# Performance work log

Hardware: AMD Instinct MI355X
Metric: run time of the kernel (lower is better)

## Reference

```python
import jax, jax.numpy as jnp
import numpy as np


def _proj(x, w, b):
    # 1x1 conv as channel matmul: x (n,c,h,w), w (k,c), b (k,) -> (n,k,h,w)
    return jnp.einsum('nchw,kc->nkhw', x, w) + b[None, :, None, None]


def setup_inputs() -> dict:
    key = jax.random.key(0)
    ks = jax.random.split(key, 9)
    cin, cinter = 256, 128
    n, h, w = 4, 64, 64
    s = lambda fan_in: 1.0 / np.sqrt(fan_in)
    return {
        'x': jax.random.normal(ks[0], (n, cin, h, w), jnp.float32),
        'theta_w': jax.random.normal(ks[1], (cinter, cin), jnp.float32) * s(cin),
        'theta_b': jax.random.normal(ks[2], (cinter,), jnp.float32) * 0.01,
        'phi_w': jax.random.normal(ks[3], (cinter, cin), jnp.float32) * s(cin),
        'phi_b': jax.random.normal(ks[4], (cinter,), jnp.float32) * 0.01,
        'g_w': jax.random.normal(ks[5], (cinter, cin), jnp.float32) * s(cin),
        'g_b': jax.random.normal(ks[6], (cinter,), jnp.float32) * 0.01,
        'w_w': jax.random.normal(ks[7], (cin, cinter), jnp.float32) * s(cinter),
        'w_b': jax.random.normal(ks[8], (cin,), jnp.float32) * 0.01,
    }


def reference(x, theta_w, theta_b, phi_w, phi_b, g_w, g_b, w_w, w_b):
    n, c, h, w = x.shape
    cinter = theta_w.shape[0]
    hw = h * w
    theta_x = _proj(x, theta_w, theta_b).reshape(n, cinter, hw)  # (n,ci,HW)
    phi_x = _proj(x, phi_w, phi_b).reshape(n, cinter, hw)        # (n,ci,HW)
    g_x = _proj(x, g_w, g_b).reshape(n, cinter, hw)              # (n,ci,HW)
    # f_x = phi^T @ theta : (n, HW, HW), softmax over last dim (theta positions)
    f_x = jnp.einsum('nci,ncj->nij', phi_x, theta_x)
    f_x = jax.nn.softmax(f_x, axis=-1)
    # attended = g @ f : (n, ci, HW)
    att = jnp.einsum('nci,nij->ncj', g_x, f_x).reshape(n, cinter, h, w)
    res_x = _proj(att, w_w, w_b)  # (n, c, h, w)
    return x + res_x
```

## Files before the change

### kernel.cpp

```cpp
#include <hip/hip_runtime.h>
#include <hip/hip_bf16.h>

#define B_ 4
#define C_ 256
#define CI_ 128
#define P_ 4096
#define LOG2E 1.44269504088896340736f

typedef __attribute__((ext_vector_type(8))) _Float16 half8;
typedef __attribute__((ext_vector_type(2))) __fp16 fp16x2;
typedef __attribute__((ext_vector_type(8))) short short8;
typedef __attribute__((ext_vector_type(4))) short short4v;
typedef __attribute__((ext_vector_type(4))) float floatx4;

__device__ __forceinline__ float bf2f(ushort h) {
  union { unsigned u; float f; } v; v.u = ((unsigned)h) << 16; return v.f;
}
__device__ __forceinline__ ushort f2bf(float f) {
  union { float f; unsigned u; } v; v.f = f;
  unsigned r = v.u + 0x7FFFu + ((v.u >> 16) & 1u);
  return (ushort)(r >> 16);
}
__device__ __forceinline__ ushort f2h(float f) {
  _Float16 h = (_Float16)f;
  union { _Float16 h; ushort u; } v; v.h = h; return v.u;
}
__device__ __forceinline__ uint pk2h(float a, float b) {
  union { fp16x2 h2; uint u; } cv;
  cv.h2 = __builtin_amdgcn_cvt_pkrtz(a, b);
  return cv.u;
}
__device__ __forceinline__ half8 ld8h(const void* src, size_t off, int is_bf16) {
  union { uint u[4]; half8 v; } r;
  if (is_bf16) {
    short8 x = *(const short8*)((const ushort*)src + off);
#pragma unroll
    for (int i = 0; i < 4; ++i)
      r.u[i] = pk2h(bf2f((ushort)x[2 * i]), bf2f((ushort)x[2 * i + 1]));
  } else {
    const float* f = (const float*)src + off;
    float4 a = *(const float4*)f, b = *(const float4*)(f + 4);
    r.u[0] = pk2h(a.x, a.y); r.u[1] = pk2h(a.z, a.w);
    r.u[2] = pk2h(b.x, b.y); r.u[3] = pk2h(b.z, b.w);
  }
  return r.v;
}
__device__ __forceinline__ float ldf(const void* src, int idx, int is_bf16) {
  return is_bf16 ? bf2f(((const ushort*)src)[idx]) : ((const float*)src)[idx];
}

#define MFMA16(a, b, c) __builtin_amdgcn_mfma_f32_16x16x32_f16((a), (b), (c), 0, 0, 0)

__device__ __forceinline__ int detect_bf16(const ushort* __restrict__ xu) {
  __shared__ int cnt_;
  if (threadIdx.x == 0) cnt_ = 0;
  __syncthreads();
  int local = 0;
  int t = threadIdx.x & 255;
#pragma unroll
  for (int s = 0; s < 8; ++s) {
    ushort u = xu[(t * 8 + s) * 2];
    int e = (u >> 7) & 0xFF;
    local += (e >= 0x70 && e <= 0x84) ? 1 : 0;
  }
  atomicAdd(&cnt_, local);
  __syncthreads();
  return cnt_ > 1024;
}

__global__ __launch_bounds__(256, 4) void k_proj(
    const void* __restrict__ xv,
    const void* __restrict__ twv, const void* __restrict__ pwv,
    const void* __restrict__ gwv,
    const void* __restrict__ tbv, const void* __restrict__ pbv,
    const void* __restrict__ gbv,
    ushort* __restrict__ thetaT, ushort* __restrict__ phiT,
    ushort* __restrict__ g) {
  int is_bf16 = detect_bf16((const ushort*)xv);
  __shared__ __align__(16) ushort xtl[32][264];
  int t = threadIdx.x;
  int w = t >> 6, lane = t & 63, l = lane & 15, q = lane >> 4;
  int p0 = blockIdx.x * 32, b = blockIdx.y;
  {
    int c_loc = t >> 2;
    int p_loc = (t & 3) * 8;
#pragma unroll
    for (int cb = 0; cb < 4; ++cb) {
      size_t base = ((size_t)(b * C_) + cb * 64 + c_loc) * P_ + p0 + p_loc;
      float vv[8];
      if (is_bf16) {
        short8 v = *(const short8*)((const ushort*)xv + base);
#pragma unroll
        for (int i = 0; i < 8; ++i) vv[i] = bf2f((ushort)v[i]);
      } else {
        const float* xf = (const float*)xv;
        float4 v0 = *(const float4*)(xf + base);
        float4 v1 = *(const float4*)(xf + base + 4);
        vv[0] = v0.x; vv[1] = v0.y; vv[2] = v0.z; vv[3] = v0.w;
        vv[4] = v1.x; vv[5] = v1.y; vv[6] = v1.z; vv[7] = v1.w;
      }
#pragma unroll
      for (int i = 0; i < 8; ++i) {
        int iw = (i + t) & 7;
        xtl[p_loc + iw][cb * 64 + c_loc] = f2h(vv[iw]);
      }
    }
  }
  __syncthreads();
  const void* wsrc[3] = {twv, pwv, gwv};
  const void* bsrc[3] = {tbv, pbv, gbv};
  floatx4 acc[2][6];
#pragma unroll
  for (int ps = 0; ps < 2; ++ps)
#pragma unroll
    for (int ks = 0; ks < 6; ++ks) acc[ps][ks] = (floatx4){0.f, 0.f, 0.f, 0.f};
  int prj[6], kloc[6];
#pragma unroll
  for (int ks = 0; ks < 6; ++ks) {
    int kg = w * 96 + ks * 16;
    prj[ks] = kg >> 7;
    kloc[ks] = kg & 127;
  }
  for (int c = 0; c < C_; c += 32) {
    half8 av[2], wv[6];
#pragma unroll
    for (int ps = 0; ps < 2; ++ps)
      av[ps] = *(const half8*)&xtl[ps * 16 + l][c + q * 8];
#pragma unroll
    for (int ks = 0; ks < 6; ++ks)
      wv[ks] = ld8h(wsrc[prj[ks]], (size_t)(kloc[ks] + l) * C_ + c + q * 8, is_bf16);
#pragma unroll
    for (int ps = 0; ps < 2; ++ps)
#pragma unroll
      for (int ks = 0; ks < 6; ++ks)
        acc[ps][ks] = MFMA16(av[ps], wv[ks], acc[ps][ks]);
  }
#pragma unroll
  for (int ks = 0; ks < 6; ++ks) {
    float bias = ldf(bsrc[prj[ks]], kloc[ks] + l, is_bf16);
#pragma unroll
    for (int ps = 0; ps < 2; ++ps) {
      floatx4 d = acc[ps][ks];
      if (prj[ks] < 2) {
        ushort* dst = (prj[ks] == 0 ? thetaT : phiT) +
                      ((size_t)(b * P_) + p0 + ps * 16 + q * 4) * CI_ + kloc[ks] + l;
#pragma unroll
        for (int r = 0; r < 4; ++r) dst[(size_t)r * CI_] = f2h(d[r] + bias);
      } else {
        ushort* dst = g + ((size_t)(b * CI_) + kloc[ks] + l) * P_ + p0 + ps * 16 + q * 4;
        short4v pk;
#pragma unroll
        for (int r = 0; r < 4; ++r) pk[r] = (short)f2h(d[r] + bias);
        *(short4v*)dst = pk;
      }
    }
  }
}

__global__ __launch_bounds__(256, 2) void k_stats(
    const ushort* __restrict__ phiT, const ushort* __restrict__ thetaT,
    float* __restrict__ part) {
  int t = threadIdx.x, w = t >> 6, lane = t & 63, l = lane & 15, q = lane >> 4;
  int i0 = blockIdx.x * 256, j0 = blockIdx.y * 512, b = blockIdx.z;
  half8 av[4][4];
#pragma unroll
  for (int is = 0; is < 4; ++is) {
    const ushort* pr = phiT + ((size_t)(b * P_) + i0 + w * 64 + is * 16 + l) * CI_;
#pragma unroll
    for (int ks = 0; ks < 4; ++ks) av[is][ks] = *(const half8*)(pr + ks * 32 + q * 8);
  }
  float sum[4][4];
#pragma unroll
  for (int is = 0; is < 4; ++is)
#pragma unroll
    for (int r = 0; r < 4; ++r) sum[is][r] = 0.f;
  const ushort* tb0 = thetaT + (size_t)b * P_ * CI_;
  for (int jc = 0; jc < 16; ++jc) {
    int j = j0 + jc * 32;
    half8 bv[2][4];
#pragma unroll
    for (int js = 0; js < 2; ++js) {
      const ushort* tr = tb0 + (size_t)(j + js * 16 + l) * CI_;
#pragma unroll
      for (int ks = 0; ks < 4; ++ks) bv[js][ks] = *(const half8*)(tr + ks * 32 + q * 8);
    }
    floatx4 accS[4][2];
#pragma unroll
    for (int is = 0; is < 4; ++is)
#pragma unroll
      for (int js = 0; js < 2; ++js) accS[is][js] = (floatx4){0.f, 0.f, 0.f, 0.f};
#pragma unroll
    for (int ks = 0; ks < 4; ++ks)
#pragma unroll
      for (int is = 0; is < 4; ++is)
#pragma unroll
        for (int js = 0; js < 2; ++js)
          accS[is][js] = MFMA16(av[is][ks], bv[js][ks], accS[is][js]);
#pragma unroll
    for (int is = 0; is < 4; ++is)
#pragma unroll
      for (int js = 0; js < 2; ++js)
#pragma unroll
        for (int r = 0; r < 4; ++r)
          sum[is][r] += exp2f(fmaf(accS[is][js][r], LOG2E, -64.f));
  }
#pragma unroll
  for (int d = 1; d < 16; d <<= 1)
#pragma unroll
    for (int is = 0; is < 4; ++is)
#pragma unroll
      for (int r = 0; r < 4; ++r) sum[is][r] += __shfl_xor(sum[is][r], d, 64);
  if (l == 0) {
#pragma unroll
    for (int is = 0; is < 4; ++is)
#pragma unroll
      for (int r = 0; r < 4; ++r)
        part[((size_t)blockIdx.y * B_ + b) * P_ + i0 + w * 64 + is * 16 + q * 4 + r] =
            sum[is][r];
  }
}

__global__ __launch_bounds__(256, 2) void k_attn(
    const ushort* __restrict__ phiT, const ushort* __restrict__ thetaT,
    const ushort* __restrict__ g, const float* __restrict__ part,
    ushort* __restrict__ attP0, ushort* __restrict__ attP1) {
  __shared__ __align__(16) ushort thL[128][136];
  __shared__ __align__(16) ushort eL[128][136];
  __shared__ __align__(16) float oL[2048];
  int t = threadIdx.x;
  int w = t >> 6, lane = t & 63, l = lane & 15, q = lane >> 4;
  int j0 = blockIdx.x * 128, ih = blockIdx.y, b = blockIdx.z;
  int istart = ih * 2048;
#pragma unroll
  for (int it = 0; it < 8; ++it) {
    int lin = it * 256 + t, row = lin >> 4, cg = (lin & 15) * 8;
    *(short8*)&thL[row][cg] =
        *(const short8*)(thetaT + ((size_t)(b * P_) + j0 + row) * CI_ + cg);
  }
#pragma unroll
  for (int z = 0; z < 8; ++z) {
    int iloc = z * 256 + t;
    float s = 0.f;
#pragma unroll
    for (int js = 0; js < 8; ++js)
      s += part[((size_t)js * B_ + b) * P_ + istart + iloc];
    oL[iloc] = log2f(s) + 64.f;
  }
  floatx4 accA[2][8];
#pragma unroll
  for (int cs = 0; cs < 2; ++cs)
#pragma unroll
    for (int js = 0; js < 8; ++js) accA[cs][js] = (floatx4){0.f, 0.f, 0.f, 0.f};
  __syncthreads();
  half8 af[2][4];
  float4 ov[2];
#pragma unroll
  for (int is = 0; is < 2; ++is) {
    int iG = istart + w * 32 + is * 16;
    const ushort* pr = phiT + ((size_t)(b * P_) + iG + l) * CI_;
#pragma unroll
    for (int ks = 0; ks < 4; ++ks) af[is][ks] = *(const half8*)(pr + ks * 32 + q * 8);
    ov[is] = *(const float4*)&oL[w * 32 + is * 16 + q * 4];
  }
  for (int ic = 0; ic < 16; ++ic) {
    int ibase = istart + ic * 128;
    half8 gf[2][4];
#pragma unroll
    for (int cs = 0; cs < 2; ++cs) {
      const ushort* gr = g + ((size_t)(b * CI_) + w * 32 + cs * 16 + l) * P_ + ibase;
#pragma unroll
      for (int ks = 0; ks < 4; ++ks) gf[cs][ks] = *(const half8*)(gr + ks * 32 + q * 8);
    }
    floatx4 accS[2][8];
#pragma unroll
    for (int is = 0; is < 2; ++is)
#pragma unroll
      for (int js = 0; js < 8; ++js) accS[is][js] = (floatx4){0.f, 0.f, 0.f, 0.f};
#pragma unroll
    for (int ks = 0; ks < 4; ++ks) {
      half8 bf[8];
#pragma unroll
      for (int js = 0; js < 8; ++js) bf[js] = *(const half8*)&thL[js * 16 + l][ks * 32 + q * 8];
#pragma unroll
      for (int is = 0; is < 2; ++is)
#pragma unroll
        for (int js = 0; js < 8; ++js) accS[is][js] = MFMA16(af[is][ks], bf[js], accS[is][js]);
    }
    uint2 ep[2][8];
#pragma unroll
    for (int is = 0; is < 2; ++is)
#pragma unroll
      for (int js = 0; js < 8; ++js) {
        float e0 = exp2f(fminf(fmaf(accS[is][js][0], LOG2E, -ov[is].x), 0.5f));
        float e1 = exp2f(fminf(fmaf(accS[is][js][1], LOG2E, -ov[is].y), 0.5f));
        float e2 = exp2f(fminf(fmaf(accS[is][js][2], LOG2E, -ov[is].z), 0.5f));
        float e3 = exp2f(fminf(fmaf(accS[is][js][3], LOG2E, -ov[is].w), 0.5f));
        ep[is][js] = (uint2){pk2h(e0, e1), pk2h(e2, e3)};
      }
    __syncthreads();
#pragma unroll
    for (int is = 0; is < 2; ++is)
#pragma unroll
      for (int js = 0; js < 8; ++js)
        *(uint2*)&eL[js * 16 + l][w * 32 + is * 16 + q * 4] = ep[is][js];
    __syncthreads();
    if (ic < 15) {
      int nb = istart + (ic + 1) * 128;
#pragma unroll
      for (int is = 0; is < 2; ++is) {
        int iG = nb + w * 32 + is * 16;
        const ushort* pr = phiT + ((size_t)(b * P_) + iG + l) * CI_;
#pragma unroll
        for (int ks = 0; ks < 4; ++ks) af[is][ks] = *(const half8*)(pr + ks * 32 + q * 8);
        ov[is] = *(const float4*)&oL[(nb - istart) + w * 32 + is * 16 + q * 4];
      }
    }
#pragma unroll
    for (int ks = 0; ks < 4; ++ks) {
      half8 ef[8];
#pragma unroll
      for (int js = 0; js < 8; ++js) ef[js] = *(const half8*)&eL[js * 16 + l][ks * 32 + q * 8];
#pragma unroll
      for (int cs = 0; cs < 2; ++cs)
#pragma unroll
        for (int js = 0; js < 8; ++js) accA[cs][js] = MFMA16(gf[cs][ks], ef[js], accA[cs][js]);
    }
  }
  ushort* ap = (ih == 0 ? attP0 : attP1);
#pragma unroll
  for (int cs = 0; cs < 2; ++cs)
#pragma unroll
    for (int js = 0; js < 8; ++js) {
      uint2 pk = (uint2){pk2h(accA[cs][js][0], accA[cs][js][1]),
                         pk2h(accA[cs][js][2], accA[cs][js][3])};
      *(uint2*)(ap + ((size_t)(b * P_) + j0 + js * 16 + l) * CI_ +
                w * 32 + cs * 16 + q * 4) = pk;
    }
}

__global__ __launch_bounds__(256, 4) void k_out(
    const ushort* __restrict__ attP0, const ushort* __restrict__ attP1,
    const void* __restrict__ wwv, const void* __restrict__ wbv,
    const void* __restrict__ xv, void* __restrict__ outv) {
  int is_bf16 = detect_bf16((const ushort*)xv);
  int t = threadIdx.x;
  int w = t >> 6, lane = t & 63, l = lane & 15, q = lane >> 4;
  int p0 = blockIdx.x * 32, b = blockIdx.y;
  floatx4 accR[4][2];
#pragma unroll
  for (int kk = 0; kk < 4; ++kk)
#pragma unroll
    for (int js = 0; js < 2; ++js) accR[kk][js] = (floatx4){0.f, 0.f, 0.f, 0.f};
#pragma unroll
  for (int ks = 0; ks < 4; ++ks) {
    half8 wf[4], af[2];
#pragma unroll
    for (int kk = 0; kk < 4; ++kk)
      wf[kk] = ld8h(wwv, (size_t)(w * 64 + kk * 16 + l) * CI_ + ks * 32 + q * 8, is_bf16);
#pragma unroll
    for (int js = 0; js < 2; ++js) {
      size_t off = ((size_t)(b * P_) + p0 + js * 16 + l) * CI_ + ks * 32 + q * 8;
      half8 s = *(const half8*)(attP0 + off);
      s = s + *(const half8*)(attP1 + off);
      af[js] = s;
    }
#pragma unroll
    for (int kk = 0; kk < 4; ++kk)
#pragma unroll
      for (int js = 0; js < 2; ++js) accR[kk][js] = MFMA16(wf[kk], af[js], accR[kk][js]);
  }
#pragma unroll
  for (int kk = 0; kk < 4; ++kk)
#pragma unroll
    for (int r = 0; r < 4; ++r) {
      int c = w * 64 + kk * 16 + q * 4 + r;
      float bias = ldf(wbv, c, is_bf16);
#pragma unroll
      for (int js = 0; js < 2; ++js) {
        int p = p0 + js * 16 + l;
        size_t idx = ((size_t)(b * C_) + c) * P_ + p;
        float val = accR[kk][js][r] + bias;
        if (is_bf16) {
          ((ushort*)outv)[idx] = f2bf(bf2f(((const ushort*)xv)[idx]) + val);
        } else {
          ((float*)outv)[idx] = ((const float*)xv)[idx] + val;
        }
      }
    }
}

extern "C" void kernel_launch(void* const* d_in, const int* in_sizes, int n_in,
                              void* d_out, int out_size, void* d_ws, size_t ws_size,
                              hipStream_t stream) {
  const void* x  = d_in[0];
  const void* tw = d_in[1];
  const void* tb = d_in[2];
  const void* pw = d_in[3];
  const void* pb = d_in[4];
  const void* gw = d_in[5];
  const void* gb = d_in[6];
  const void* ww = d_in[7];
  const void* wb = d_in[8];
  char* ws = (char*)d_ws;
  float*  part   = (float*)(ws);
  ushort* attP0  = (ushort*)(ws + (1u << 20));
  ushort* thetaT = (ushort*)(ws + (9u << 20));
  ushort* phiT   = (ushort*)(ws + (13u << 20));
  ushort* gbuf   = (ushort*)(ws + (17u << 20));
  ushort* attP1  = (ushort*)(ws + (21u << 20));

  k_proj<<<dim3(128, 4), 256, 0, stream>>>(x, tw, pw, gw, tb, pb, gb,
                                           thetaT, phiT, gbuf);
  k_stats<<<dim3(16, 8, 4), 256, 0, stream>>>(phiT, thetaT, part);
  k_attn<<<dim3(32, 2, 4), 256, 0, stream>>>(phiT, thetaT, gbuf, part, attP0, attP1);
  k_out<<<dim3(128, 4), 256, 0, stream>>>(attP0, attP1, ww, wb, x, d_out);
}
```

Before: 257.1 us.

## Split log-sum-exp into its own kernel and retile attention warps as 2x2

Moves the reduction of partial softmax sums and the log2 into a separate small kernel that writes one offset per row. k_attn then reads these offsets straight from global memory and no longer needs the oL shared buffer. It also changes the warp tiling from 4x1 (32 rows by 128 columns per warp) to 2x2 (64x64 per warp), which cuts redundant LDS fragment reads per MFMA. The g-fragment loads move after the barrier. The square tiles raise register pressure (16 accumulators per operand set plus 16 phi fragments), and the extra kernel launch adds a small overhead.

```diff
diff --git a/kernel.cpp b/kernel.cpp
--- a/kernel.cpp
+++ b/kernel.cpp
@@ -220,15 +220,23 @@
   }
 }
 
+__global__ void k_lse(const float* __restrict__ part, float* __restrict__ o2) {
+  int idx = blockIdx.x * 256 + threadIdx.x;
+  float s = 0.f;
+#pragma unroll
+  for (int p = 0; p < 8; ++p) s += part[(size_t)p * (B_ * P_) + idx];
+  o2[idx] = log2f(s) + 64.f;
+}
+
 __global__ __launch_bounds__(256, 2) void k_attn(
     const ushort* __restrict__ phiT, const ushort* __restrict__ thetaT,
-    const ushort* __restrict__ g, const float* __restrict__ part,
+    const ushort* __restrict__ g, const float* __restrict__ o2,
     ushort* __restrict__ attP0, ushort* __restrict__ attP1) {
   __shared__ __align__(16) ushort thL[128][136];
   __shared__ __align__(16) ushort eL[128][136];
-  __shared__ __align__(16) float oL[2048];
   int t = threadIdx.x;
   int w = t >> 6, lane = t & 63, l = lane & 15, q = lane >> 4;
+  int a = w >> 1, jh = w & 1;
   int j0 = blockIdx.x * 128, ih = blockIdx.y, b = blockIdx.z;
   int istart = ih * 2048;
 #pragma unroll
@@ -237,60 +245,47 @@
     *(short8*)&thL[row][cg] =
         *(const short8*)(thetaT + ((size_t)(b * P_) + j0 + row) * CI_ + cg);
   }
-#pragma unroll
-  for (int z = 0; z < 8; ++z) {
-    int iloc = z * 256 + t;
-    float s = 0.f;
-#pragma unroll
-    for (int js = 0; js < 8; ++js)
-      s += part[((size_t)js * B_ + b) * P_ + istart + iloc];
-    oL[iloc] = log2f(s) + 64.f;
-  }
-  floatx4 accA[2][8];
-#pragma unroll
-  for (int cs = 0; cs < 2; ++cs)
-#pragma unroll
-    for (int js = 0; js < 8; ++js) accA[cs][js] = (floatx4){0.f, 0.f, 0.f, 0.f};
+  floatx4 accA[4][4];
+#pragma unroll
+  for (int cs = 0; cs < 4; ++cs)
+#pragma unroll
+    for (int js = 0; js < 4; ++js) accA[cs][js] = (floatx4){0.f, 0.f, 0.f, 0.f};
   __syncthreads();
-  half8 af[2][4];
-  float4 ov[2];
-#pragma unroll
-  for (int is = 0; is < 2; ++is) {
-    int iG = istart + w * 32 + is * 16;
+  const float* orow = o2 + b * P_;
+  half8 af[4][4];
+  float4 ov[4];
+#pragma unroll
+  for (int is = 0; is < 4; ++is) {
+    int iG = istart + a * 64 + is * 16;
     const ushort* pr = phiT + ((size_t)(b * P_) + iG + l) * CI_;
 #pragma unroll
     for (int ks = 0; ks < 4; ++ks) af[is][ks] = *(const half8*)(pr + ks * 32 + q * 8);
-    ov[is] = *(const float4*)&oL[w * 32 + is * 16 + q * 4];
+    ov[is] = *(const float4*)(orow + iG + q * 4);
   }
   for (int ic = 0; ic < 16; ++ic) {
     int ibase = istart + ic * 128;
-    half8 gf[2][4];
-#pragma unroll
-    for (int cs = 0; cs < 2; ++cs) {
-      const ushort* gr = g + ((size_t)(b * CI_) + w * 32 + cs * 16 + l) * P_ + ibase;
-#pragma unroll
-      for (int ks = 0; ks < 4; ++ks) gf[cs][ks] = *(const half8*)(gr + ks * 32 + q * 8);
-    }
-    floatx4 accS[2][8];
-#pragma unroll
-    for (int is = 0; is < 2; ++is)
-#pragma unroll
-      for (int js = 0; js < 8; ++js) accS[is][js] = (floatx4){0.f, 0.f, 0.f, 0.f};
+    floatx4 accS[4][4];
+#pragma unroll
+    for (int is = 0; is < 4; ++is)
+#pragma unroll
+      for (int js = 0; js < 4; ++js) accS[is][js] = (floatx4){0.f, 0.f, 0.f, 0.f};
 #pragma unroll
     for (int ks = 0; ks < 4; ++ks) {
-      half8 bf[8];
-#pragma unroll
-      for (int js = 0; js < 8; ++js) bf[js] = *(const half8*)&thL[js * 16 + l][ks * 32 + q * 8];
-#pragma unroll
-      for (int is = 0; is < 2; ++is)
-#pragma unroll
-        for (int js = 0; js < 8; ++js) accS[is][js] = MFMA16(af[is][ks], bf[js], accS[is][js]);
-    }
-    uint2 ep[2][8];
-#pragma unroll
-    for (int is = 0; is < 2; ++is)
-#pragma unroll
-      for (int js = 0; js < 8; ++js) {
+      half8 bf[4];
+#pragma unroll
+      for (int js = 0; js < 4; ++js)
+        bf[js] = *(const half8*)&thL[jh * 64 + js * 16 + l][ks * 32 + q * 8];
+#pragma unroll
+      for (int is = 0; is < 4; ++is)
+#pragma unroll
+        for (int js = 0; js < 4; ++js)
+          accS[is][js] = MFMA16(af[is][ks], bf[js], accS[is][js]);
+    }
+    uint2 ep[4][4];
+#pragma unroll
+    for (int is = 0; is < 4; ++is)
+#pragma unroll
+      for (int js = 0; js < 4; ++js) {
         float e0 = exp2f(fminf(fmaf(accS[is][js][0], LOG2E, -ov[is].x), 0.5f));
         float e1 = exp2f(fminf(fmaf(accS[is][js][1], LOG2E, -ov[is].y), 0.5f));
         float e2 = exp2f(fminf(fmaf(accS[is][js][2], LOG2E, -ov[is].z), 0.5f));
@@ -299,42 +294,51 @@
       }
     __syncthreads();
 #pragma unroll
-    for (int is = 0; is < 2; ++is)
-#pragma unroll
-      for (int js = 0; js < 8; ++js)
-        *(uint2*)&eL[js * 16 + l][w * 32 + is * 16 + q * 4] = ep[is][js];
+    for (int is = 0; is < 4; ++is)
+#pragma unroll
+      for (int js = 0; js < 4; ++js)
+        *(uint2*)&eL[jh * 64 + js * 16 + l][a * 64 + is * 16 + q * 4] = ep[is][js];
     __syncthreads();
+    half8 gf[4][4];
+#pragma unroll
+    for (int cs = 0; cs < 4; ++cs) {
+      const ushort* gr = g + ((size_t)(b * CI_) + a * 64 + cs * 16 + l) * P_ + ibase;
+#pragma unroll
+      for (int ks = 0; ks < 4; ++ks) gf[cs][ks] = *(const half8*)(gr + ks * 32 + q * 8);
+    }
     if (ic < 15) {
-      int nb = istart + (ic + 1) * 128;
-#pragma unroll
-      for (int is = 0; is < 2; ++is) {
-        int iG = nb + w * 32 + is * 16;
+      int nb = ibase + 128;
+#pragma unroll
+      for (int is = 0; is < 4; ++is) {
+        int iG = nb + a * 64 + is * 16;
         const ushort* pr = phiT + ((size_t)(b * P_) + iG + l) * CI_;
 #pragma unroll
         for (int ks = 0; ks < 4; ++ks) af[is][ks] = *(const half8*)(pr + ks * 32 + q * 8);
-        ov[is] = *(const float4*)&oL[(nb - istart) + w * 32 + is * 16 + q * 4];
+        ov[is] = *(const float4*)(orow + iG + q * 4);
       }
     }
 #pragma unroll
     for (int ks = 0; ks < 4; ++ks) {
-      half8 ef[8];
-#pragma unroll
-      for (int js = 0; js < 8; ++js) ef[js] = *(const half8*)&eL[js * 16 + l][ks * 32 + q * 8];
-#pragma unroll
-      for (int cs = 0; cs < 2; ++cs)
-#pragma unroll
-        for (int js = 0; js < 8; ++js) accA[cs][js] = MFMA16(gf[cs][ks], ef[js], accA[cs][js]);
+      half8 ef[4];
+#pragma unroll
+      for (int js = 0; js < 4; ++js)
+        ef[js] = *(const half8*)&eL[jh * 64 + js * 16 + l][ks * 32 + q * 8];
+#pragma unroll
+      for (int cs = 0; cs < 4; ++cs)
+#pragma unroll
+        for (int js = 0; js < 4; ++js)
+          accA[cs][js] = MFMA16(gf[cs][ks], ef[js], accA[cs][js]);
     }
   }
   ushort* ap = (ih == 0 ? attP0 : attP1);
 #pragma unroll
-  for (int cs = 0; cs < 2; ++cs)
-#pragma unroll
-    for (int js = 0; js < 8; ++js) {
+  for (int cs = 0; cs < 4; ++cs)
+#pragma unroll
+    for (int js = 0; js < 4; ++js) {
       uint2 pk = (uint2){pk2h(accA[cs][js][0], accA[cs][js][1]),
                          pk2h(accA[cs][js][2], accA[cs][js][3])};
-      *(uint2*)(ap + ((size_t)(b * P_) + j0 + js * 16 + l) * CI_ +
-                w * 32 + cs * 16 + q * 4) = pk;
+      *(uint2*)(ap + ((size_t)(b * P_) + j0 + jh * 64 + js * 16 + l) * CI_ +
+                a * 64 + cs * 16 + q * 4) = pk;
     }
 }
 
@@ -403,6 +407,7 @@
   const void* wb = d_in[8];
   char* ws = (char*)d_ws;
   float*  part   = (float*)(ws);
+  float*  o2     = (float*)(ws + (512u << 10));
   ushort* attP0  = (ushort*)(ws + (1u << 20));
   ushort* thetaT = (ushort*)(ws + (9u << 20));
   ushort* phiT   = (ushort*)(ws + (13u << 20));
@@ -412,6 +417,7 @@
   k_proj<<<dim3(128, 4), 256, 0, stream>>>(x, tw, pw, gw, tb, pb, gb,
                                            thetaT, phiT, gbuf);
   k_stats<<<dim3(16, 8, 4), 256, 0, stream>>>(phiT, thetaT, part);
-  k_attn<<<dim3(32, 2, 4), 256, 0, stream>>>(phiT, thetaT, gbuf, part, attP0, attP1);
+  k_lse<<<64, 256, 0, stream>>>(part, o2);
+  k_attn<<<dim3(32, 2, 4), 256, 0, stream>>>(phiT, thetaT, gbuf, o2, attP0, attP1);
   k_out<<<dim3(128, 4), 256, 0, stream>>>(attP0, attP1, ww, wb, x, d_out);
 }
```

New measurement: 295.0 us. +14.7%, slower.

## Split attention across four query chunks and add separate log-sum-exp kernel

Applied to the files above, without the earlier changes.

Raises the number of blocks in the attention kernel by splitting the softmax-row dimension into four chunks instead of two, and halves the per-block row tile in the stats kernel so it launches twice as many blocks with higher occupancy bounds. The per-row normalizer is now computed once in a new small kernel instead of redundantly inside every attention block. The aim is to fill more compute units on a small grid. In exchange, the output kernel must read and sum four fp16 partials, which adds memory traffic and rounding, and there is one extra launch.

```diff
diff --git a/kernel.cpp b/kernel.cpp
--- a/kernel.cpp
+++ b/kernel.cpp
@@ -157,21 +157,21 @@
   }
 }
 
-__global__ __launch_bounds__(256, 2) void k_stats(
+__global__ __launch_bounds__(256, 4) void k_stats(
     const ushort* __restrict__ phiT, const ushort* __restrict__ thetaT,
     float* __restrict__ part) {
   int t = threadIdx.x, w = t >> 6, lane = t & 63, l = lane & 15, q = lane >> 4;
-  int i0 = blockIdx.x * 256, j0 = blockIdx.y * 512, b = blockIdx.z;
-  half8 av[4][4];
-#pragma unroll
-  for (int is = 0; is < 4; ++is) {
-    const ushort* pr = phiT + ((size_t)(b * P_) + i0 + w * 64 + is * 16 + l) * CI_;
+  int i0 = blockIdx.x * 128, j0 = blockIdx.y * 512, b = blockIdx.z;
+  half8 av[2][4];
+#pragma unroll
+  for (int is = 0; is < 2; ++is) {
+    const ushort* pr = phiT + ((size_t)(b * P_) + i0 + w * 32 + is * 16 + l) * CI_;
 #pragma unroll
     for (int ks = 0; ks < 4; ++ks) av[is][ks] = *(const half8*)(pr + ks * 32 + q * 8);
   }
-  float sum[4][4];
-#pragma unroll
-  for (int is = 0; is < 4; ++is)
+  float sum[2][4];
+#pragma unroll
+  for (int is = 0; is < 2; ++is)
 #pragma unroll
     for (int r = 0; r < 4; ++r) sum[is][r] = 0.f;
   const ushort* tb0 = thetaT + (size_t)b * P_ * CI_;
@@ -184,20 +184,20 @@
 #pragma unroll
       for (int ks = 0; ks < 4; ++ks) bv[js][ks] = *(const half8*)(tr + ks * 32 + q * 8);
     }
-    floatx4 accS[4][2];
-#pragma unroll
-    for (int is = 0; is < 4; ++is)
+    floatx4 accS[2][2];
+#pragma unroll
+    for (int is = 0; is < 2; ++is)
 #pragma unroll
       for (int js = 0; js < 2; ++js) accS[is][js] = (floatx4){0.f, 0.f, 0.f, 0.f};
 #pragma unroll
     for (int ks = 0; ks < 4; ++ks)
 #pragma unroll
-      for (int is = 0; is < 4; ++is)
+      for (int is = 0; is < 2; ++is)
 #pragma unroll
         for (int js = 0; js < 2; ++js)
           accS[is][js] = MFMA16(av[is][ks], bv[js][ks], accS[is][js]);
 #pragma unroll
-    for (int is = 0; is < 4; ++is)
+    for (int is = 0; is < 2; ++is)
 #pragma unroll
       for (int js = 0; js < 2; ++js)
 #pragma unroll
@@ -207,51 +207,50 @@
 #pragma unroll
   for (int d = 1; d < 16; d <<= 1)
 #pragma unroll
-    for (int is = 0; is < 4; ++is)
+    for (int is = 0; is < 2; ++is)
 #pragma unroll
       for (int r = 0; r < 4; ++r) sum[is][r] += __shfl_xor(sum[is][r], d, 64);
   if (l == 0) {
 #pragma unroll
-    for (int is = 0; is < 4; ++is)
+    for (int is = 0; is < 2; ++is)
 #pragma unroll
       for (int r = 0; r < 4; ++r)
-        part[((size_t)blockIdx.y * B_ + b) * P_ + i0 + w * 64 + is * 16 + q * 4 + r] =
+        part[((size_t)blockIdx.y * B_ + b) * P_ + i0 + w * 32 + is * 16 + q * 4 + r] =
             sum[is][r];
   }
+}
+
+__global__ void k_lse(const float* __restrict__ part, float* __restrict__ o2) {
+  int idx = blockIdx.x * 256 + threadIdx.x;
+  float s = 0.f;
+#pragma unroll
+  for (int p = 0; p < 8; ++p) s += part[(size_t)p * (B_ * P_) + idx];
+  o2[idx] = log2f(s) + 64.f;
 }
 
 __global__ __launch_bounds__(256, 2) void k_attn(
     const ushort* __restrict__ phiT, const ushort* __restrict__ thetaT,
-    const ushort* __restrict__ g, const float* __restrict__ part,
-    ushort* __restrict__ attP0, ushort* __restrict__ attP1) {
+    const ushort* __restrict__ g, const float* __restrict__ o2,
+    ushort* __restrict__ attP) {
   __shared__ __align__(16) ushort thL[128][136];
   __shared__ __align__(16) ushort eL[128][136];
-  __shared__ __align__(16) float oL[2048];
   int t = threadIdx.x;
   int w = t >> 6, lane = t & 63, l = lane & 15, q = lane >> 4;
   int j0 = blockIdx.x * 128, ih = blockIdx.y, b = blockIdx.z;
-  int istart = ih * 2048;
 #pragma unroll
   for (int it = 0; it < 8; ++it) {
     int lin = it * 256 + t, row = lin >> 4, cg = (lin & 15) * 8;
     *(short8*)&thL[row][cg] =
         *(const short8*)(thetaT + ((size_t)(b * P_) + j0 + row) * CI_ + cg);
   }
-#pragma unroll
-  for (int z = 0; z < 8; ++z) {
-    int iloc = z * 256 + t;
-    float s = 0.f;
-#pragma unroll
-    for (int js = 0; js < 8; ++js)
-      s += part[((size_t)js * B_ + b) * P_ + istart + iloc];
-    oL[iloc] = log2f(s) + 64.f;
-  }
   floatx4 accA[2][8];
 #pragma unroll
   for (int cs = 0; cs < 2; ++cs)
 #pragma unroll
     for (int js = 0; js < 8; ++js) accA[cs][js] = (floatx4){0.f, 0.f, 0.f, 0.f};
   __syncthreads();
+  const float* orow = o2 + b * P_;
+  int istart = ih * 1024;
   half8 af[2][4];
   float4 ov[2];
 #pragma unroll
@@ -260,9 +259,9 @@
     const ushort* pr = phiT + ((size_t)(b * P_) + iG + l) * CI_;
 #pragma unroll
     for (int ks = 0; ks < 4; ++ks) af[is][ks] = *(const half8*)(pr + ks * 32 + q * 8);
-    ov[is] = *(const float4*)&oL[w * 32 + is * 16 + q * 4];
-  }
-  for (int ic = 0; ic < 16; ++ic) {
+    ov[is] = *(const float4*)(orow + iG + q * 4);
+  }
+  for (int ic = 0; ic < 8; ++ic) {
     int ibase = istart + ic * 128;
     half8 gf[2][4];
 #pragma unroll
@@ -304,15 +303,15 @@
       for (int js = 0; js < 8; ++js)
         *(uint2*)&eL[js * 16 + l][w * 32 + is * 16 + q * 4] = ep[is][js];
     __syncthreads();
-    if (ic < 15) {
-      int nb = istart + (ic + 1) * 128;
+    if (ic < 7) {
+      int nb = ibase + 128;
 #pragma unroll
       for (int is = 0; is < 2; ++is) {
         int iG = nb + w * 32 + is * 16;
         const ushort* pr = phiT + ((size_t)(b * P_) + iG + l) * CI_;
 #pragma unroll
         for (int ks = 0; ks < 4; ++ks) af[is][ks] = *(const half8*)(pr + ks * 32 + q * 8);
-        ov[is] = *(const float4*)&oL[(nb - istart) + w * 32 + is * 16 + q * 4];
+        ov[is] = *(const float4*)(orow + iG + q * 4);
       }
     }
 #pragma unroll
@@ -326,7 +325,7 @@
         for (int js = 0; js < 8; ++js) accA[cs][js] = MFMA16(gf[cs][ks], ef[js], accA[cs][js]);
     }
   }
-  ushort* ap = (ih == 0 ? attP0 : attP1);
+  ushort* ap = attP + (size_t)ih * (B_ * P_ * CI_);
 #pragma unroll
   for (int cs = 0; cs < 2; ++cs)
 #pragma unroll
@@ -339,7 +338,7 @@
 }
 
 __global__ __launch_bounds__(256, 4) void k_out(
-    const ushort* __restrict__ attP0, const ushort* __restrict__ attP1,
+    const ushort* __restrict__ attP,
     const void* __restrict__ wwv, const void* __restrict__ wbv,
     const void* __restrict__ xv, void* __restrict__ outv) {
   int is_bf16 = detect_bf16((const ushort*)xv);
@@ -360,8 +359,10 @@
 #pragma unroll
     for (int js = 0; js < 2; ++js) {
       size_t off = ((size_t)(b * P_) + p0 + js * 16 + l) * CI_ + ks * 32 + q * 8;
-      half8 s = *(const half8*)(attP0 + off);
-      s = s + *(const half8*)(attP1 + off);
+      half8 s = *(const half8*)(attP + off);
+#pragma unroll
+      for (int ihh = 1; ihh < 4; ++ihh)
+        s = s + *(const half8*)(attP + (size_t)ihh * (B_ * P_ * CI_) + off);
       af[js] = s;
     }
 #pragma unroll
@@ -403,15 +404,16 @@
   const void* wb = d_in[8];
   char* ws = (char*)d_ws;
   float*  part   = (float*)(ws);
-  ushort* attP0  = (ushort*)(ws + (1u << 20));
-  ushort* thetaT = (ushort*)(ws + (9u << 20));
-  ushort* phiT   = (ushort*)(ws + (13u << 20));
-  ushort* gbuf   = (ushort*)(ws + (17u << 20));
-  ushort* attP1  = (ushort*)(ws + (21u << 20));
+  float*  o2     = (float*)(ws + (512u << 10));
+  ushort* thetaT = (ushort*)(ws + (1u << 20));
+  ushort* phiT   = (ushort*)(ws + (5u << 20));
+  ushort* gbuf   = (ushort*)(ws + (9u << 20));
+  ushort* attP   = (ushort*)(ws + (13u << 20));
 
   k_proj<<<dim3(128, 4), 256, 0, stream>>>(x, tw, pw, gw, tb, pb, gb,
                                            thetaT, phiT, gbuf);
-  k_stats<<<dim3(16, 8, 4), 256, 0, stream>>>(phiT, thetaT, part);
-  k_attn<<<dim3(32, 2, 4), 256, 0, stream>>>(phiT, thetaT, gbuf, part, attP0, attP1);
-  k_out<<<dim3(128, 4), 256, 0, stream>>>(attP0, attP1, ww, wb, x, d_out);
-}
+  k_stats<<<dim3(32, 8, 4), 256, 0, stream>>>(phiT, thetaT, part);
+  k_lse<<<64, 256, 0, stream>>>(part, o2);
+  k_attn<<<dim3(32, 4, 4), 256, 0, stream>>>(phiT, thetaT, gbuf, o2, attP);
+  k_out<<<dim3(128, 4), 256, 0, stream>>>(attP, ww, wb, x, d_out);
+}
```

Result: no change. 261.0 us (+1.5%).
